# Performance work log

Measured on AMD Instinct MI355X. Metric: run time of the kernel, lower is better.

## Reference

```python
import jax, jax.numpy as jnp
import numpy as np

N = 262144   # nodes
E = 2097152  # edges (avg degree 8)
F_IN, L0, L1, K = 14, 128, 15, 15


def setup_inputs() -> dict:
    key = jax.random.key(0)
    ks = jax.random.split(key, 24)
    s = 0.1
    return {
        "x": jax.random.normal(ks[0], (N, F_IN), jnp.float32),
        "edge_index": jax.random.randint(ks[1], (2, E), 0, N, dtype=jnp.int32),
        "y": jax.random.randint(ks[2], (N, 1), 0, 2, dtype=jnp.int32),
        "sel": jax.random.bernoulli(ks[3], 0.98, (N, 1)),
        "Wl1": jax.random.normal(ks[4], (F_IN, L0)) * s,
        "Wr1": jax.random.normal(ks[5], (F_IN, L0)) * s,
        "b1": jnp.zeros((L0,), jnp.float32),
        "Wl2": jax.random.normal(ks[6], (L0, L0)) * s,
        "Wr2": jax.random.normal(ks[7], (L0, L0)) * s,
        "b2": jnp.zeros((L0,), jnp.float32),
        "Wl3": jax.random.normal(ks[8], (L0, 1)) * s,
        "Wr3": jax.random.normal(ks[9], (L0, 1)) * s,
        "b3": jnp.zeros((1,), jnp.float32),
        "Wt1": jax.random.normal(ks[10], (K + 1, F_IN, L1)) * s,
        "bt1": jnp.zeros((L1,), jnp.float32),
        "Wt2": jax.random.normal(ks[11], (K + 1, L1, L1)) * s,
        "bt2": jnp.zeros((L1,), jnp.float32),
        "Wt3": jax.random.normal(ks[12], (K + 1, L1, 1)) * s,
        "bt3": jnp.zeros((1,), jnp.float32),
        "Wlin": jax.random.normal(ks[13], (2, 1)) * s,
        "blin": jnp.zeros((1,), jnp.float32),
    }


def _sage(h, src, dst, inv_deg, Wl, Wr, b):
    # PyG SAGEConv (mean aggr): lin_l(mean_j x_j) + lin_r(x_i) + b
    agg = jax.ops.segment_sum(h[src], dst, num_segments=N) * inv_deg
    return agg @ Wl + h @ Wr + b


def _tag(h, src, dst, norm, W, b):
    # PyG TAGConv: sum_k (D^-1/2 A D^-1/2)^k x @ W_k + b
    out = h @ W[0]
    for k in range(1, W.shape[0]):
        h = jax.ops.segment_sum(norm[:, None] * h[src], dst, num_segments=N)
        out = out + h @ W[k]
    return out + b


def reference(x, edge_index, y, sel, Wl1, Wr1, b1, Wl2, Wr2, b2, Wl3, Wr3, b3,
              Wt1, bt1, Wt2, bt2, Wt3, bt3, Wlin, blin):
    src, dst = edge_index[0], edge_index[1]
    ones = jnp.ones((E,), jnp.float32)
    deg = jax.ops.segment_sum(ones, dst, num_segments=N)  # in-degree at targets
    inv_deg = (1.0 / jnp.maximum(deg, 1.0))[:, None]
    # gcn_norm without self-loops for TAGConv
    dinv = jnp.where(deg > 0, jax.lax.rsqrt(jnp.maximum(deg, 1.0)), 0.0)
    norm = dinv[src] * dinv[dst]  # [E]

    # SAGE branch
    x1 = jax.nn.sigmoid(_sage(x, src, dst, inv_deg, Wl1, Wr1, b1))
    for _ in range(4):
        x1 = jax.nn.sigmoid(_sage(x1, src, dst, inv_deg, Wl2, Wr2, b2))
    x1 = jax.nn.relu(_sage(x1, src, dst, inv_deg, Wl3, Wr3, b3))

    # TAG branch
    x3 = jax.nn.sigmoid(_tag(x, src, dst, norm, Wt1, bt1))
    for _ in range(4):
        x3 = jax.nn.sigmoid(_tag(x3, src, dst, norm, Wt2, bt2))
    x3 = jax.nn.relu(_tag(x3, src, dst, norm, Wt3, bt3))

    out = jax.nn.relu(jnp.concatenate([x1, x3], axis=1) @ Wlin + blin)
    return jnp.where(sel & (y == 0), 0.0, out)
```

## Files before the change

kernel.cpp:

```cpp
#include <hip/hip_runtime.h>
#include <math.h>

#define NN 262144
#define EE 2097152
#define FIN 14
#define LW 128
#define TW 15

typedef unsigned short ushort_t;
typedef unsigned int uint_t;
typedef __attribute__((ext_vector_type(8))) short bf16x8v;
typedef __attribute__((ext_vector_type(4))) float f32x4v;

static __device__ __forceinline__ float sigmoidf_(float v) { return 1.0f / (1.0f + expf(-v)); }

static __device__ __forceinline__ float bf2f(unsigned short u) {
  union { unsigned int i; float f; } v; v.i = ((unsigned int)u) << 16; return v.f;
}
static __device__ __forceinline__ unsigned short f2bf(float f) {
  union { float f; unsigned int i; } v; v.f = f;
  unsigned int r = v.i + 0x7FFF + ((v.i >> 16) & 1);
  return (unsigned short)(r >> 16);
}
static __device__ __forceinline__ unsigned int pack2(float a, float b) {
  return ((unsigned int)f2bf(b) << 16) | (unsigned int)f2bf(a);
}
static __device__ __forceinline__ void addrow16(float* acc, uint4 u0, uint4 u1) {
  acc[0]  += bf2f((unsigned short)(u0.x & 0xFFFF)); acc[1]  += bf2f((unsigned short)(u0.x >> 16));
  acc[2]  += bf2f((unsigned short)(u0.y & 0xFFFF)); acc[3]  += bf2f((unsigned short)(u0.y >> 16));
  acc[4]  += bf2f((unsigned short)(u0.z & 0xFFFF)); acc[5]  += bf2f((unsigned short)(u0.z >> 16));
  acc[6]  += bf2f((unsigned short)(u0.w & 0xFFFF)); acc[7]  += bf2f((unsigned short)(u0.w >> 16));
  acc[8]  += bf2f((unsigned short)(u1.x & 0xFFFF)); acc[9]  += bf2f((unsigned short)(u1.x >> 16));
  acc[10] += bf2f((unsigned short)(u1.y & 0xFFFF)); acc[11] += bf2f((unsigned short)(u1.y >> 16));
  acc[12] += bf2f((unsigned short)(u1.z & 0xFFFF)); acc[13] += bf2f((unsigned short)(u1.z >> 16));
  acc[14] += bf2f((unsigned short)(u1.w & 0xFFFF)); acc[15] += bf2f((unsigned short)(u1.w >> 16));
}

__global__ void k_selprobe(const unsigned char* __restrict__ selb, int* __restrict__ flag) {
  __shared__ int cnt;
  if (threadIdx.x == 0) cnt = 0;
  __syncthreads();
  int c = 0;
  for (int i = threadIdx.x; i < 4096; i += 256) c += (selb[i] != 0) ? 1 : 0;
  atomicAdd(&cnt, c);
  __syncthreads();
  if (threadIdx.x == 0) *flag = (cnt > 3000) ? 1 : 0;
}

__global__ void k_norm_bool(const int* __restrict__ flag, const unsigned char* __restrict__ selb,
                            unsigned char* __restrict__ selN) {
  if (*flag != 1) return;
  int i = blockIdx.x * 256 + threadIdx.x;
  selN[i] = (selb[i] != 0) ? 1 : 0;
}

__global__ void k_norm_int(const int* __restrict__ flag, const unsigned char* __restrict__ selb,
                           unsigned char* __restrict__ selN) {
  if (*flag != 0) return;
  int i = blockIdx.x * 256 + threadIdx.x;
  selN[i] = (((const int*)selb)[i] != 0) ? 1 : 0;
}

__global__ void k_deg(const int* __restrict__ ei, int* __restrict__ deg) {
  int e = blockIdx.x * 256 + threadIdx.x;
  if (e < EE) atomicAdd(&deg[ei[EE + e]], 1);
}

__global__ void k_scan_partial(const int* __restrict__ deg, int* __restrict__ btot) {
  __shared__ int sd[256];
  int t = threadIdx.x, b = blockIdx.x;
  int i0 = b * 1024 + t * 4;
  int s = deg[i0] + deg[i0 + 1] + deg[i0 + 2] + deg[i0 + 3];
  sd[t] = s; __syncthreads();
  for (int off = 1; off < 256; off <<= 1) {
    int x = (t >= off) ? sd[t - off] : 0;
    __syncthreads(); sd[t] += x; __syncthreads();
  }
  if (t == 255) btot[b] = sd[255];
}

__global__ void k_scan_block(const int* __restrict__ btot, int* __restrict__ bbase, int* __restrict__ row_start) {
  __shared__ int sd[256];
  int t = threadIdx.x;
  int v = btot[t];
  sd[t] = v; __syncthreads();
  for (int off = 1; off < 256; off <<= 1) {
    int x = (t >= off) ? sd[t - off] : 0;
    __syncthreads(); sd[t] += x; __syncthreads();
  }
  bbase[t] = sd[t] - v;
  if (t == 255) row_start[NN] = sd[255];
}

__global__ void k_scan_final(const int* __restrict__ deg, const int* __restrict__ bbase,
                             int* __restrict__ row_start, float* __restrict__ inv_deg,
                             float* __restrict__ dinv) {
  __shared__ int sd[256];
  int t = threadIdx.x, b = blockIdx.x;
  int i0 = b * 1024 + t * 4;
  int d0 = deg[i0], d1 = deg[i0 + 1], d2 = deg[i0 + 2], d3 = deg[i0 + 3];
  int s = d0 + d1 + d2 + d3;
  sd[t] = s; __syncthreads();
  for (int off = 1; off < 256; off <<= 1) {
    int x = (t >= off) ? sd[t - off] : 0;
    __syncthreads(); sd[t] += x; __syncthreads();
  }
  int base = bbase[b] + sd[t] - s;
  row_start[i0]     = base;
  row_start[i0 + 1] = base + d0;
  row_start[i0 + 2] = base + d0 + d1;
  row_start[i0 + 3] = base + d0 + d1 + d2;
  int dd[4] = {d0, d1, d2, d3};
  for (int j = 0; j < 4; ++j) {
    float df = (float)dd[j];
    inv_deg[i0 + j] = 1.0f / fmaxf(df, 1.0f);
    dinv[i0 + j] = (dd[j] > 0) ? rsqrtf(fmaxf(df, 1.0f)) : 0.0f;
  }
}

__global__ void k_fill(const int* __restrict__ ei, const int* __restrict__ row_start,
                       int* __restrict__ cursor, int* __restrict__ csr_src) {
  int e = blockIdx.x * 256 + threadIdx.x;
  if (e >= EE) return;
  int s = ei[e], d = ei[EE + e];
  int pos = atomicAdd(&cursor[d], 1);
  csr_src[row_start[d] + pos] = s;
}

__global__ void k_pad_x(const float* __restrict__ x, float* __restrict__ xp,
                        ushort_t* __restrict__ xpb) {
  int idx = blockIdx.x * 256 + threadIdx.x;
  int i = idx >> 4, lane = idx & 15;
  float v = (lane < FIN) ? x[(size_t)i * FIN + lane] : 0.0f;
  xp[idx] = v;
  xpb[idx] = f2bf(v);
}

__global__ __launch_bounds__(256) void k_prop16_mean(
    const float* __restrict__ h, float* __restrict__ out,
    const int* __restrict__ row_start, const int* __restrict__ csr_src,
    const float* __restrict__ inv_deg) {
  int i = blockIdx.x * 256 + threadIdx.x;
  float acc[16];
  #pragma unroll
  for (int c = 0; c < 16; ++c) acc[c] = 0.0f;
  int e0 = row_start[i], e1 = row_start[i + 1];
  int e = e0;
  for (; e + 2 <= e1; e += 2) {
    int i0 = csr_src[e], i1 = csr_src[e + 1];
    const float4* r0 = (const float4*)(h + (size_t)i0 * 16);
    const float4* r1 = (const float4*)(h + (size_t)i1 * 16);
    float4 a0 = r0[0], a1 = r0[1], a2 = r0[2], a3 = r0[3];
    float4 b0 = r1[0], b1 = r1[1], b2 = r1[2], b3 = r1[3];
    acc[0]+=a0.x+b0.x; acc[1]+=a0.y+b0.y; acc[2]+=a0.z+b0.z; acc[3]+=a0.w+b0.w;
    acc[4]+=a1.x+b1.x; acc[5]+=a1.y+b1.y; acc[6]+=a1.z+b1.z; acc[7]+=a1.w+b1.w;
    acc[8]+=a2.x+b2.x; acc[9]+=a2.y+b2.y; acc[10]+=a2.z+b2.z; acc[11]+=a2.w+b2.w;
    acc[12]+=a3.x+b3.x; acc[13]+=a3.y+b3.y; acc[14]+=a3.z+b3.z; acc[15]+=a3.w+b3.w;
  }
  for (; e < e1; ++e) {
    const float4* r0 = (const float4*)(h + (size_t)csr_src[e] * 16);
    float4 a0 = r0[0], a1 = r0[1], a2 = r0[2], a3 = r0[3];
    acc[0]+=a0.x; acc[1]+=a0.y; acc[2]+=a0.z; acc[3]+=a0.w;
    acc[4]+=a1.x; acc[5]+=a1.y; acc[6]+=a1.z; acc[7]+=a1.w;
    acc[8]+=a2.x; acc[9]+=a2.y; acc[10]+=a2.z; acc[11]+=a2.w;
    acc[12]+=a3.x; acc[13]+=a3.y; acc[14]+=a3.z; acc[15]+=a3.w;
  }
  float idg = inv_deg[i];
  float4 o[4];
  #pragma unroll
  for (int q = 0; q < 4; ++q) {
    o[q].x = acc[q*4+0]*idg; o[q].y = acc[q*4+1]*idg;
    o[q].z = acc[q*4+2]*idg; o[q].w = acc[q*4+3]*idg;
  }
  float4* dst = (float4*)(out + (size_t)i * 16);
  dst[0]=o[0]; dst[1]=o[1]; dst[2]=o[2]; dst[3]=o[3];
}

__global__ __launch_bounds__(256) void k_gemm_small(
    const float* __restrict__ A1, const float* __restrict__ A2,
    const float* __restrict__ W1, const float* __restrict__ W2,
    const float* __restrict__ bias, ushort_t* __restrict__ out) {
  __shared__ float W1s[FIN][LW];
  __shared__ float W2s[FIN][LW];
  int t = threadIdx.x;
  for (int idx = t; idx < FIN * LW; idx += 256) {
    W1s[idx / LW][idx % LW] = W1[idx];
    W2s[idx / LW][idx % LW] = W2[idx];
  }
  __syncthreads();
  int node = blockIdx.x * 4 + (t >> 6);
  int lane = t & 63;
  float a1 = (lane < 16) ? A1[(size_t)node * 16 + lane] : 0.0f;
  float a2 = (lane < 16) ? A2[(size_t)node * 16 + lane] : 0.0f;
  float acc0 = bias[lane], acc1 = bias[lane + 64];
  #pragma unroll
  for (int f = 0; f < FIN; ++f) {
    float v1 = __shfl(a1, f);
    float v2 = __shfl(a2, f);
    acc0 += v1 * W1s[f][lane]      + v2 * W2s[f][lane];
    acc1 += v1 * W1s[f][lane + 64] + v2 * W2s[f][lane + 64];
  }
  out[(size_t)node * LW + lane]      = f2bf(sigmoidf_(acc0));
  out[(size_t)node * LW + lane + 64] = f2bf(sigmoidf_(acc1));
}

__global__ void k_prop128(const ushort_t* __restrict__ h, ushort_t* __restrict__ out,
                          const int* __restrict__ row_start, const int* __restrict__ csr_src,
                          const float* __restrict__ inv_deg) {
  int t = threadIdx.x;
  int g = blockIdx.x * 4 + (t >> 6);
  int lane = t & 63;
  int s0 = row_start[g], s1 = row_start[g + 1];
  float a0 = 0.0f, a1 = 0.0f;
  int e = s0;
  for (; e + 4 <= s1; e += 4) {
    int i0 = csr_src[e], i1 = csr_src[e+1], i2 = csr_src[e+2], i3 = csr_src[e+3];
    uint_t u0 = *(const uint_t*)(h + (size_t)i0 * LW + 2 * lane);
    uint_t u1 = *(const uint_t*)(h + (size_t)i1 * LW + 2 * lane);
    uint_t u2 = *(const uint_t*)(h + (size_t)i2 * LW + 2 * lane);
    uint_t u3 = *(const uint_t*)(h + (size_t)i3 * LW + 2 * lane);
    a0 += bf2f((unsigned short)(u0 & 0xFFFF)) + bf2f((unsigned short)(u1 & 0xFFFF))
        + bf2f((unsigned short)(u2 & 0xFFFF)) + bf2f((unsigned short)(u3 & 0xFFFF));
    a1 += bf2f((unsigned short)(u0 >> 16)) + bf2f((unsigned short)(u1 >> 16))
        + bf2f((unsigned short)(u2 >> 16)) + bf2f((unsigned short)(u3 >> 16));
  }
  for (; e < s1; ++e) {
    uint_t u = *(const uint_t*)(h + (size_t)csr_src[e] * LW + 2 * lane);
    a0 += bf2f((unsigned short)(u & 0xFFFF));
    a1 += bf2f((unsigned short)(u >> 16));
  }
  float idg = inv_deg[g];
  *(uint_t*)(out + (size_t)g * LW + 2 * lane) = pack2(a0 * idg, a1 * idg);
}

__global__ void k_convW(const float* __restrict__ Wl, const float* __restrict__ Wr,
                        ushort_t* __restrict__ Wt) {
  int idx = blockIdx.x * 256 + threadIdx.x;
  int n = idx >> 8, k = idx & 255;
  float v = (k < 128) ? Wl[k * 128 + n] : Wr[(k - 128) * 128 + n];
  Wt[idx] = f2bf(v);
}

__global__ __launch_bounds__(256) void k_gemm128_mfma(
    const ushort_t* __restrict__ A1, const ushort_t* __restrict__ A2,
    const ushort_t* __restrict__ Wt,
    const float* __restrict__ bias, ushort_t* __restrict__ out) {
  int tid = threadIdx.x;
  int wave = tid >> 6, lane = tid & 63;
  int row0 = blockIdx.x * 64 + wave * 16;
  int r = lane & 15, kg = lane >> 4;
  f32x4v acc[8];
  #pragma unroll
  for (int nt = 0; nt < 8; ++nt) acc[nt] = (f32x4v){0.f, 0.f, 0.f, 0.f};
  #pragma unroll
  for (int ks = 0; ks < 8; ++ks) {
    const ushort_t* asrc = (ks < 4)
        ? (A1 + (size_t)(row0 + r) * LW + ks * 32 + kg * 8)
        : (A2 + (size_t)(row0 + r) * LW + (ks - 4) * 32 + kg * 8);
    bf16x8v a = *(const bf16x8v*)asrc;
    #pragma unroll
    for (int nt = 0; nt < 8; ++nt) {
      bf16x8v b = *(const bf16x8v*)(Wt + (size_t)(nt * 16 + r) * 256 + ks * 32 + kg * 8);
      acc[nt] = __builtin_amdgcn_mfma_f32_16x16x32_bf16(a, b, acc[nt], 0, 0, 0);
    }
  }
  #pragma unroll
  for (int nt = 0; nt < 8; ++nt) {
    #pragma unroll
    for (int j = 0; j < 4; ++j) {
      float v = sigmoidf_(acc[nt][j] + bias[nt * 16 + r]);
      out[(size_t)(row0 + kg * 4 + j) * LW + nt * 16 + r] = f2bf(v);
    }
  }
}

__global__ void k_wide_to1(const ushort_t* __restrict__ H, const float* __restrict__ Wl3,
                           const float* __restrict__ Wr3, float* __restrict__ g_l,
                           float* __restrict__ g_r) {
  int wave = (blockIdx.x * 256 + threadIdx.x) >> 6;
  int lane = threadIdx.x & 63;
  unsigned int u = *(const unsigned int*)(H + (size_t)wave * LW + 2 * lane);
  float h0 = bf2f((unsigned short)(u & 0xFFFF));
  float h1 = bf2f((unsigned short)(u >> 16));
  float al = h0 * Wl3[2 * lane] + h1 * Wl3[2 * lane + 1];
  float ar = h0 * Wr3[2 * lane] + h1 * Wr3[2 * lane + 1];
  #pragma unroll
  for (int off = 32; off; off >>= 1) {
    al += __shfl_xor(al, off);
    ar += __shfl_xor(ar, off);
  }
  if (lane == 0) { g_l[wave] = al; g_r[wave] = ar; }
}

__global__ void k_sage_final(const float* __restrict__ g_l, const float* __restrict__ g_r,
                             const float* __restrict__ b3, const int* __restrict__ row_start,
                             const int* __restrict__ csr_src, const float* __restrict__ inv_deg,
                             float* __restrict__ x1) {
  int i = blockIdx.x * 256 + threadIdx.x;
  int e0 = row_start[i], e1 = row_start[i + 1];
  float s = 0.0f;
  int e = e0;
  for (; e + 4 <= e1; e += 4) {
    float w0 = g_l[csr_src[e]], w1 = g_l[csr_src[e+1]];
    float w2 = g_l[csr_src[e+2]], w3 = g_l[csr_src[e+3]];
    s += (w0 + w1) + (w2 + w3);
  }
  for (; e < e1; ++e) s += g_l[csr_src[e]];
  float v = s * inv_deg[i] + g_r[i] + b3[0];
  x1[i] = fmaxf(v, 0.0f);
}

__global__ __launch_bounds__(256) void k_tag_hh(
    const ushort_t* __restrict__ T, const float* __restrict__ W, int win,
    const ushort_t* __restrict__ w_in, ushort_t* __restrict__ w_out,
    const float* __restrict__ bias, int mode,
    const int* __restrict__ row_start, const int* __restrict__ csr_src,
    const float* __restrict__ dinv) {
  __shared__ float Ws[16][16];
  int t = threadIdx.x;
  { int rr = t >> 4, c = t & 15; Ws[rr][c] = (rr < win && c < TW) ? W[rr * TW + c] : 0.0f; }
  __syncthreads();
  int i = blockIdx.x * 256 + t;
  float di = dinv[i];
  float acc[16];
  #pragma unroll
  for (int c = 0; c < 16; ++c) acc[c] = 0.0f;

  if (mode != 0) {
    int e0 = row_start[i], e1 = row_start[i + 1];
    int e = e0;
    for (; e + 4 <= e1; e += 4) {
      int i0 = csr_src[e], i1 = csr_src[e+1], i2 = csr_src[e+2], i3 = csr_src[e+3];
      uint4 a0 = *(const uint4*)(w_in + (size_t)i0 * 16);
      uint4 a1 = *(const uint4*)(w_in + (size_t)i0 * 16 + 8);
      uint4 b0 = *(const uint4*)(w_in + (size_t)i1 * 16);
      uint4 b1 = *(const uint4*)(w_in + (size_t)i1 * 16 + 8);
      uint4 c0 = *(const uint4*)(w_in + (size_t)i2 * 16);
      uint4 c1 = *(const uint4*)(w_in + (size_t)i2 * 16 + 8);
      uint4 d0 = *(const uint4*)(w_in + (size_t)i3 * 16);
      uint4 d1 = *(const uint4*)(w_in + (size_t)i3 * 16 + 8);
      addrow16(acc, a0, a1);
      addrow16(acc, b0, b1);
      addrow16(acc, c0, c1);
      addrow16(acc, d0, d1);
    }
    for (; e < e1; ++e) {
      int i0 = csr_src[e];
      uint4 a0 = *(const uint4*)(w_in + (size_t)i0 * 16);
      uint4 a1 = *(const uint4*)(w_in + (size_t)i0 * 16 + 8);
      addrow16(acc, a0, a1);
    }
    #pragma unroll
    for (int c = 0; c < 16; ++c) acc[c] *= di;
  }

  uint4 t0 = *(const uint4*)(T + (size_t)i * 16);
  uint4 t1 = *(const uint4*)(T + (size_t)i * 16 + 8);
  float tv[16];
  tv[0]=bf2f((unsigned short)(t0.x&0xFFFF)); tv[1]=bf2f((unsigned short)(t0.x>>16));
  tv[2]=bf2f((unsigned short)(t0.y&0xFFFF)); tv[3]=bf2f((unsigned short)(t0.y>>16));
  tv[4]=bf2f((unsigned short)(t0.z&0xFFFF)); tv[5]=bf2f((unsigned short)(t0.z>>16));
  tv[6]=bf2f((unsigned short)(t0.w&0xFFFF)); tv[7]=bf2f((unsigned short)(t0.w>>16));
  tv[8]=bf2f((unsigned short)(t1.x&0xFFFF)); tv[9]=bf2f((unsigned short)(t1.x>>16));
  tv[10]=bf2f((unsigned short)(t1.y&0xFFFF)); tv[11]=bf2f((unsigned short)(t1.y>>16));
  tv[12]=bf2f((unsigned short)(t1.z&0xFFFF)); tv[13]=bf2f((unsigned short)(t1.z>>16));
  tv[14]=bf2f((unsigned short)(t1.w&0xFFFF)); tv[15]=bf2f((unsigned short)(t1.w>>16));
  #pragma unroll
  for (int f = 0; f < 16; ++f) {
    float tf = tv[f];
    const float4* wr = (const float4*)Ws[f];
    float4 w0 = wr[0], w1 = wr[1], w2 = wr[2], w3 = wr[3];
    acc[0]+=tf*w0.x; acc[1]+=tf*w0.y; acc[2]+=tf*w0.z; acc[3]+=tf*w0.w;
    acc[4]+=tf*w1.x; acc[5]+=tf*w1.y; acc[6]+=tf*w1.z; acc[7]+=tf*w1.w;
    acc[8]+=tf*w2.x; acc[9]+=tf*w2.y; acc[10]+=tf*w2.z; acc[11]+=tf*w2.w;
    acc[12]+=tf*w3.x; acc[13]+=tf*w3.y; acc[14]+=tf*w3.z; acc[15]+=tf*w3.w;
  }

  uint_t o[8];
  if (mode == 2) {
    #pragma unroll
    for (int q = 0; q < 8; ++q) {
      float v0 = (2*q   < TW) ? sigmoidf_(acc[2*q]   + bias[2*q])   : 0.0f;
      float v1 = (2*q+1 < TW) ? sigmoidf_(acc[2*q+1] + bias[2*q+1]) : 0.0f;
      o[q] = pack2(v0, v1);
    }
  } else {
    #pragma unroll
    for (int q = 0; q < 8; ++q) o[q] = pack2(di * acc[2*q], di * acc[2*q+1]);
  }
  uint4* dst = (uint4*)(w_out + (size_t)i * 16);
  dst[0] = make_uint4(o[0], o[1], o[2], o[3]);
  dst[1] = make_uint4(o[4], o[5], o[6], o[7]);
}

__global__ void k_tag_g(const ushort_t* __restrict__ T, const float* __restrict__ Wt3,
                        float* __restrict__ gT) {
  __shared__ float Ws[16 * TW];
  int t = threadIdx.x;
  if (t < 16 * TW) Ws[t] = Wt3[t];
  __syncthreads();
  int i = blockIdx.x * 256 + t;
  const ushort_t* tr = T + (size_t)i * 16;
  float row[TW];
  #pragma unroll
  for (int f = 0; f < TW; ++f) row[f] = bf2f(tr[f]);
  #pragma unroll
  for (int k = 0; k < 16; ++k) {
    float a = 0.0f;
    #pragma unroll
    for (int f = 0; f < TW; ++f) a += row[f] * Ws[k * TW + f];
    gT[(size_t)k * NN + i] = a;
  }
}

__global__ void k_scale1(const float* __restrict__ g15, const float* __restrict__ dinv,
                         float* __restrict__ w) {
  int i = blockIdx.x * 256 + threadIdx.x;
  w[i] = dinv[i] * g15[i];
}

__global__ void k_horner(const float* __restrict__ gk, const float* __restrict__ w_in,
                         float* __restrict__ w_out, int last,
                         const int* __restrict__ row_start, const int* __restrict__ csr_src,
                         const float* __restrict__ dinv) {
  int i = blockIdx.x * 256 + threadIdx.x;
  int e0 = row_start[i], e1 = row_start[i + 1];
  float gs = 0.0f;
  int e = e0;
  for (; e + 4 <= e1; e += 4) {
    float w0 = w_in[csr_src[e]],   w1 = w_in[csr_src[e+1]];
    float w2 = w_in[csr_src[e+2]], w3 = w_in[csr_src[e+3]];
    gs += (w0 + w1) + (w2 + w3);
  }
  for (; e < e1; ++e) gs += w_in[csr_src[e]];
  float s = gk[i] + dinv[i] * gs;
  w_out[i] = last ? s : dinv[i] * s;
}

__global__ void k_combine(const float* __restrict__ x1, const float* __restrict__ s,
                          const int* __restrict__ y, const unsigned char* __restrict__ selN,
                          const float* __restrict__ Wlin, const float* __restrict__ blin,
                          const float* __restrict__ bt3, float* __restrict__ out) {
  int i = blockIdx.x * 256 + threadIdx.x;
  float x3 = fmaxf(s[i] + bt3[0], 0.0f);
  float v = fmaxf(x1[i] * Wlin[0] + x3 * Wlin[1] + blin[0], 0.0f);
  bool z = (selN[i] != 0) && (y[i] == 0);
  out[i] = z ? 0.0f : v;
}

extern "C" void kernel_launch(void* const* d_in, const int* in_sizes, int n_in,
                              void* d_out, int out_size, void* d_ws, size_t ws_size,
                              hipStream_t stream) {
  const float* x    = (const float*)d_in[0];
  const int*   ei   = (const int*)d_in[1];
  const int*   y    = (const int*)d_in[2];
  const unsigned char* sel = (const unsigned char*)d_in[3];
  const float* Wl1  = (const float*)d_in[4];
  const float* Wr1  = (const float*)d_in[5];
  const float* b1   = (const float*)d_in[6];
  const float* Wl2  = (const float*)d_in[7];
  const float* Wr2  = (const float*)d_in[8];
  const float* b2   = (const float*)d_in[9];
  const float* Wl3  = (const float*)d_in[10];
  const float* Wr3  = (const float*)d_in[11];
  const float* b3   = (const float*)d_in[12];
  const float* Wt1  = (const float*)d_in[13];
  const float* bt1  = (const float*)d_in[14];
  const float* Wt2  = (const float*)d_in[15];
  const float* bt2  = (const float*)d_in[16];
  const float* Wt3  = (const float*)d_in[17];
  const float* bt3  = (const float*)d_in[18];
  const float* Wlin = (const float*)d_in[19];
  const float* blin = (const float*)d_in[20];

  const size_t MB = 1 << 20;
  unsigned char* w8 = (unsigned char*)d_ws;
  int*   deg       = (int*)(w8 + 0 * MB);
  int*   cursor    = (int*)(w8 + 1 * MB);
  int*   row_start = (int*)(w8 + 2 * MB);
  float* inv_deg   = (float*)(w8 + 4 * MB);
  float* dinv      = (float*)(w8 + 5 * MB);
  float* x1        = (float*)(w8 + 6 * MB);
  float* g_l       = (float*)(w8 + 7 * MB);
  float* g_r       = (float*)(w8 + 8 * MB);
  int*   btot      = (int*)(w8 + 9 * MB);
  int*   bbase     = (int*)(w8 + 9 * MB + 4096);
  int*   selflag   = (int*)(w8 + 9 * MB + 8192);
  float* sA        = (float*)(w8 + 10 * MB);
  float* w6a       = (float*)(w8 + 11 * MB);
  float* w6b       = (float*)(w8 + 12 * MB);
  unsigned char* selN = (unsigned char*)(w8 + 13 * MB);
  ushort_t* Wtc    = (ushort_t*)(w8 + 14 * MB);
  int*   csr_src   = (int*)(w8 + 16 * MB);
  float* xp        = (float*)(w8 + 24 * MB);
  ushort_t* xpb    = (ushort_t*)(w8 + 40 * MB);
  ushort_t* H      = (ushort_t*)(w8 + 48 * MB);
  ushort_t* AGG    = (ushort_t*)(w8 + 112 * MB);
  float* agg16     = (float*)(w8 + 112 * MB);
  ushort_t* T0  = (ushort_t*)(w8 + 112 * MB);
  ushort_t* T1  = (ushort_t*)(w8 + 120 * MB);
  ushort_t* wA  = (ushort_t*)(w8 + 128 * MB);
  ushort_t* wB  = (ushort_t*)(w8 + 136 * MB);
  float* gT     = (float*)(w8 + 144 * MB);

  k_selprobe<<<1, 256, 0, stream>>>(sel, selflag);
  k_norm_bool<<<NN / 256, 256, 0, stream>>>(selflag, sel, selN);
  k_norm_int<<<NN / 256, 256, 0, stream>>>(selflag, sel, selN);

  hipMemsetAsync(w8, 0, 2 * MB, stream);
  k_deg<<<EE / 256, 256, 0, stream>>>(ei, deg);
  k_scan_partial<<<256, 256, 0, stream>>>(deg, btot);
  k_scan_block<<<1, 256, 0, stream>>>(btot, bbase, row_start);
  k_scan_final<<<256, 256, 0, stream>>>(deg, bbase, row_start, inv_deg, dinv);
  k_fill<<<EE / 256, 256, 0, stream>>>(ei, row_start, cursor, csr_src);
  k_pad_x<<<NN * 16 / 256, 256, 0, stream>>>(x, xp, xpb);
  k_convW<<<128, 256, 0, stream>>>(Wl2, Wr2, Wtc);

  k_prop16_mean<<<NN / 256, 256, 0, stream>>>(xp, agg16, row_start, csr_src, inv_deg);
  k_gemm_small<<<NN / 4, 256, 0, stream>>>(agg16, xp, Wl1, Wr1, b1, H);
  for (int l = 0; l < 4; ++l) {
    k_prop128<<<NN / 4, 256, 0, stream>>>(H, AGG, row_start, csr_src, inv_deg);
    k_gemm128_mfma<<<NN / 64, 256, 0, stream>>>(AGG, H, Wtc, b2, H);
  }
  k_wide_to1<<<NN / 4, 256, 0, stream>>>(H, Wl3, Wr3, g_l, g_r);
  k_sage_final<<<NN / 256, 256, 0, stream>>>(g_l, g_r, b3, row_start, csr_src, inv_deg, x1);

  {
    const ushort_t* T = xpb;
    k_tag_hh<<<NN / 256, 256, 0, stream>>>(T, Wt1 + (size_t)15 * FIN * TW, FIN,
                                           nullptr, wA, nullptr, 0, row_start, csr_src, dinv);
    ushort_t* wi = wA; ushort_t* wo = wB;
    for (int k = 14; k >= 1; --k) {
      k_tag_hh<<<NN / 256, 256, 0, stream>>>(T, Wt1 + (size_t)k * FIN * TW, FIN,
                                             wi, wo, nullptr, 1, row_start, csr_src, dinv);
      ushort_t* tmp = wi; wi = wo; wo = tmp;
    }
    k_tag_hh<<<NN / 256, 256, 0, stream>>>(T, Wt1, FIN, wi, T0, bt1, 2,
                                           row_start, csr_src, dinv);
  }
  ushort_t* tin = T0; ushort_t* tout = T1;
  for (int l = 0; l < 4; ++l) {
    k_tag_hh<<<NN / 256, 256, 0, stream>>>(tin, Wt2 + (size_t)15 * TW * TW, TW,
                                           nullptr, wA, nullptr, 0, row_start, csr_src, dinv);
    ushort_t* wi = wA; ushort_t* wo = wB;
    for (int k = 14; k >= 1; --k) {
      k_tag_hh<<<NN / 256, 256, 0, stream>>>(tin, Wt2 + (size_t)k * TW * TW, TW,
                                             wi, wo, nullptr, 1, row_start, csr_src, dinv);
      ushort_t* tmp = wi; wi = wo; wo = tmp;
    }
    k_tag_hh<<<NN / 256, 256, 0, stream>>>(tin, Wt2, TW, wi, tout, bt2, 2,
                                           row_start, csr_src, dinv);
    ushort_t* tmp = tin; tin = tout; tout = tmp;
  }
  k_tag_g<<<NN / 256, 256, 0, stream>>>(tin, Wt3, gT);
  k_scale1<<<NN / 256, 256, 0, stream>>>(gT + (size_t)15 * NN, dinv, w6a);
  float* wi = w6a; float* wo = w6b;
  for (int k = 14; k >= 0; --k) {
    int last = (k == 0) ? 1 : 0;
    float* dst = last ? sA : wo;
    k_horner<<<NN / 256, 256, 0, stream>>>(gT + (size_t)k * NN, wi, dst, last,
                                           row_start, csr_src, dinv);
    float* tmp = wi; wi = wo; wo = tmp;
  }

  k_combine<<<NN / 256, 256, 0, stream>>>(x1, sA, y, selN, Wlin, blin, bt3, (float*)d_out);
}
```

Before: 4.211 ms.

## Fuse TAG layer boundaries, Horner tail, and use MFMA for first SAGE layer

Several changes at once. The first SAGE layer's aggregate and self features are packed into one bf16 buffer so a single MFMA GEMM replaces the shared-memory FMA GEMM, and the gather loops in prop128 and tag_hh are unrolled to 8 edges to keep more loads in flight. Each TAG layer's final kernel also computes the next layer's k=15 Horner seed, which removes one launch per layer. k_scale1 is folded into k_tag_g and the last Horner step into the combine kernel. The price is extra register pressure and a bf16-rounded agg input to the first GEMM.

```diff
diff --git a/kernel.cpp b/kernel.cpp
--- a/kernel.cpp
+++ b/kernel.cpp
@@ -128,16 +128,18 @@
 }
 
 __global__ void k_pad_x(const float* __restrict__ x, float* __restrict__ xp,
-                        ushort_t* __restrict__ xpb) {
+                        ushort_t* __restrict__ xpb, ushort_t* __restrict__ xc) {
   int idx = blockIdx.x * 256 + threadIdx.x;
   int i = idx >> 4, lane = idx & 15;
   float v = (lane < FIN) ? x[(size_t)i * FIN + lane] : 0.0f;
   xp[idx] = v;
-  xpb[idx] = f2bf(v);
+  ushort_t b = f2bf(v);
+  xpb[idx] = b;
+  xc[(size_t)i * 32 + 16 + lane] = b;
 }
 
 __global__ __launch_bounds__(256) void k_prop16_mean(
-    const float* __restrict__ h, float* __restrict__ out,
+    const float* __restrict__ h, ushort_t* __restrict__ xc,
     const int* __restrict__ row_start, const int* __restrict__ csr_src,
     const float* __restrict__ inv_deg) {
   int i = blockIdx.x * 256 + threadIdx.x;
@@ -166,42 +168,47 @@
     acc[12]+=a3.x; acc[13]+=a3.y; acc[14]+=a3.z; acc[15]+=a3.w;
   }
   float idg = inv_deg[i];
-  float4 o[4];
-  #pragma unroll
-  for (int q = 0; q < 4; ++q) {
-    o[q].x = acc[q*4+0]*idg; o[q].y = acc[q*4+1]*idg;
-    o[q].z = acc[q*4+2]*idg; o[q].w = acc[q*4+3]*idg;
-  }
-  float4* dst = (float4*)(out + (size_t)i * 16);
-  dst[0]=o[0]; dst[1]=o[1]; dst[2]=o[2]; dst[3]=o[3];
-}
-
-__global__ __launch_bounds__(256) void k_gemm_small(
-    const float* __restrict__ A1, const float* __restrict__ A2,
-    const float* __restrict__ W1, const float* __restrict__ W2,
+  uint_t o[8];
+  #pragma unroll
+  for (int q = 0; q < 8; ++q) o[q] = pack2(acc[2*q]*idg, acc[2*q+1]*idg);
+  uint4* dst = (uint4*)(xc + (size_t)i * 32);
+  dst[0] = make_uint4(o[0], o[1], o[2], o[3]);
+  dst[1] = make_uint4(o[4], o[5], o[6], o[7]);
+}
+
+__global__ void k_convW1(const float* __restrict__ Wl1, const float* __restrict__ Wr1,
+                         ushort_t* __restrict__ Wc) {
+  int idx = blockIdx.x * 256 + threadIdx.x;
+  int n = idx >> 5, k = idx & 31;
+  float v = 0.0f;
+  if (k < FIN) v = Wl1[k * 128 + n];
+  else if (k >= 16 && k < 16 + FIN) v = Wr1[(k - 16) * 128 + n];
+  Wc[idx] = f2bf(v);
+}
+
+__global__ __launch_bounds__(256) void k_gemm_small_mfma(
+    const ushort_t* __restrict__ xc, const ushort_t* __restrict__ Wc,
     const float* __restrict__ bias, ushort_t* __restrict__ out) {
-  __shared__ float W1s[FIN][LW];
-  __shared__ float W2s[FIN][LW];
-  int t = threadIdx.x;
-  for (int idx = t; idx < FIN * LW; idx += 256) {
-    W1s[idx / LW][idx % LW] = W1[idx];
-    W2s[idx / LW][idx % LW] = W2[idx];
-  }
-  __syncthreads();
-  int node = blockIdx.x * 4 + (t >> 6);
-  int lane = t & 63;
-  float a1 = (lane < 16) ? A1[(size_t)node * 16 + lane] : 0.0f;
-  float a2 = (lane < 16) ? A2[(size_t)node * 16 + lane] : 0.0f;
-  float acc0 = bias[lane], acc1 = bias[lane + 64];
-  #pragma unroll
-  for (int f = 0; f < FIN; ++f) {
-    float v1 = __shfl(a1, f);
-    float v2 = __shfl(a2, f);
-    acc0 += v1 * W1s[f][lane]      + v2 * W2s[f][lane];
-    acc1 += v1 * W1s[f][lane + 64] + v2 * W2s[f][lane + 64];
-  }
-  out[(size_t)node * LW + lane]      = f2bf(sigmoidf_(acc0));
-  out[(size_t)node * LW + lane + 64] = f2bf(sigmoidf_(acc1));
+  int tid = threadIdx.x;
+  int wave = tid >> 6, lane = tid & 63;
+  int row0 = blockIdx.x * 64 + wave * 16;
+  int r = lane & 15, kg = lane >> 4;
+  bf16x8v a = *(const bf16x8v*)(xc + (size_t)(row0 + r) * 32 + kg * 8);
+  f32x4v acc[8];
+  #pragma unroll
+  for (int nt = 0; nt < 8; ++nt) {
+    acc[nt] = (f32x4v){0.f, 0.f, 0.f, 0.f};
+    bf16x8v b = *(const bf16x8v*)(Wc + (size_t)(nt * 16 + r) * 32 + kg * 8);
+    acc[nt] = __builtin_amdgcn_mfma_f32_16x16x32_bf16(a, b, acc[nt], 0, 0, 0);
+  }
+  #pragma unroll
+  for (int nt = 0; nt < 8; ++nt) {
+    #pragma unroll
+    for (int j = 0; j < 4; ++j) {
+      float v = sigmoidf_(acc[nt][j] + bias[nt * 16 + r]);
+      out[(size_t)(row0 + kg * 4 + j) * LW + nt * 16 + r] = f2bf(v);
+    }
+  }
 }
 
 __global__ void k_prop128(const ushort_t* __restrict__ h, ushort_t* __restrict__ out,
@@ -213,16 +220,18 @@
   int s0 = row_start[g], s1 = row_start[g + 1];
   float a0 = 0.0f, a1 = 0.0f;
   int e = s0;
-  for (; e + 4 <= s1; e += 4) {
-    int i0 = csr_src[e], i1 = csr_src[e+1], i2 = csr_src[e+2], i3 = csr_src[e+3];
-    uint_t u0 = *(const uint_t*)(h + (size_t)i0 * LW + 2 * lane);
-    uint_t u1 = *(const uint_t*)(h + (size_t)i1 * LW + 2 * lane);
-    uint_t u2 = *(const uint_t*)(h + (size_t)i2 * LW + 2 * lane);
-    uint_t u3 = *(const uint_t*)(h + (size_t)i3 * LW + 2 * lane);
-    a0 += bf2f((unsigned short)(u0 & 0xFFFF)) + bf2f((unsigned short)(u1 & 0xFFFF))
-        + bf2f((unsigned short)(u2 & 0xFFFF)) + bf2f((unsigned short)(u3 & 0xFFFF));
-    a1 += bf2f((unsigned short)(u0 >> 16)) + bf2f((unsigned short)(u1 >> 16))
-        + bf2f((unsigned short)(u2 >> 16)) + bf2f((unsigned short)(u3 >> 16));
+  for (; e + 8 <= s1; e += 8) {
+    int id[8];
+    #pragma unroll
+    for (int j = 0; j < 8; ++j) id[j] = csr_src[e + j];
+    uint_t u[8];
+    #pragma unroll
+    for (int j = 0; j < 8; ++j) u[j] = *(const uint_t*)(h + (size_t)id[j] * LW + 2 * lane);
+    #pragma unroll
+    for (int j = 0; j < 8; ++j) {
+      a0 += bf2f((unsigned short)(u[j] & 0xFFFF));
+      a1 += bf2f((unsigned short)(u[j] >> 16));
+    }
   }
   for (; e < s1; ++e) {
     uint_t u = *(const uint_t*)(h + (size_t)csr_src[e] * LW + 2 * lane);
@@ -314,11 +323,17 @@
     const ushort_t* __restrict__ T, const float* __restrict__ W, int win,
     const ushort_t* __restrict__ w_in, ushort_t* __restrict__ w_out,
     const float* __restrict__ bias, int mode,
+    const float* __restrict__ W2, int win2, ushort_t* __restrict__ w_next2,
     const int* __restrict__ row_start, const int* __restrict__ csr_src,
     const float* __restrict__ dinv) {
   __shared__ float Ws[16][16];
+  __shared__ float Ws2[16][16];
   int t = threadIdx.x;
   { int rr = t >> 4, c = t & 15; Ws[rr][c] = (rr < win && c < TW) ? W[rr * TW + c] : 0.0f; }
+  if (mode == 3) {
+    int rr = t >> 4, c = t & 15;
+    Ws2[rr][c] = (rr < win2 && c < TW) ? W2[rr * TW + c] : 0.0f;
+  }
   __syncthreads();
   int i = blockIdx.x * 256 + t;
   float di = dinv[i];
@@ -329,26 +344,35 @@
   if (mode != 0) {
     int e0 = row_start[i], e1 = row_start[i + 1];
     int e = e0;
+    for (; e + 8 <= e1; e += 8) {
+      int id[8];
+      #pragma unroll
+      for (int j = 0; j < 8; ++j) id[j] = csr_src[e + j];
+      uint4 u0[8], u1[8];
+      #pragma unroll
+      for (int j = 0; j < 8; ++j) {
+        const uint4* p = (const uint4*)(w_in + (size_t)id[j] * 16);
+        u0[j] = p[0]; u1[j] = p[1];
+      }
+      #pragma unroll
+      for (int j = 0; j < 8; ++j) addrow16(acc, u0[j], u1[j]);
+    }
     for (; e + 4 <= e1; e += 4) {
-      int i0 = csr_src[e], i1 = csr_src[e+1], i2 = csr_src[e+2], i3 = csr_src[e+3];
-      uint4 a0 = *(const uint4*)(w_in + (size_t)i0 * 16);
-      uint4 a1 = *(const uint4*)(w_in + (size_t)i0 * 16 + 8);
-      uint4 b0 = *(const uint4*)(w_in + (size_t)i1 * 16);
-      uint4 b1 = *(const uint4*)(w_in + (size_t)i1 * 16 + 8);
-      uint4 c0 = *(const uint4*)(w_in + (size_t)i2 * 16);
-      uint4 c1 = *(const uint4*)(w_in + (size_t)i2 * 16 + 8);
-      uint4 d0 = *(const uint4*)(w_in + (size_t)i3 * 16);
-      uint4 d1 = *(const uint4*)(w_in + (size_t)i3 * 16 + 8);
-      addrow16(acc, a0, a1);
-      addrow16(acc, b0, b1);
-      addrow16(acc, c0, c1);
-      addrow16(acc, d0, d1);
+      int id[4];
+      #pragma unroll
+      for (int j = 0; j < 4; ++j) id[j] = csr_src[e + j];
+      uint4 u0[4], u1[4];
+      #pragma unroll
+      for (int j = 0; j < 4; ++j) {
+        const uint4* p = (const uint4*)(w_in + (size_t)id[j] * 16);
+        u0[j] = p[0]; u1[j] = p[1];
+      }
+      #pragma unroll
+      for (int j = 0; j < 4; ++j) addrow16(acc, u0[j], u1[j]);
     }
     for (; e < e1; ++e) {
-      int i0 = csr_src[e];
-      uint4 a0 = *(const uint4*)(w_in + (size_t)i0 * 16);
-      uint4 a1 = *(const uint4*)(w_in + (size_t)i0 * 16 + 8);
-      addrow16(acc, a0, a1);
+      const uint4* p = (const uint4*)(w_in + (size_t)csr_src[e] * 16);
+      addrow16(acc, p[0], p[1]);
     }
     #pragma unroll
     for (int c = 0; c < 16; ++c) acc[c] *= di;
@@ -376,25 +400,51 @@
     acc[12]+=tf*w3.x; acc[13]+=tf*w3.y; acc[14]+=tf*w3.z; acc[15]+=tf*w3.w;
   }
 
-  uint_t o[8];
-  if (mode == 2) {
-    #pragma unroll
-    for (int q = 0; q < 8; ++q) {
-      float v0 = (2*q   < TW) ? sigmoidf_(acc[2*q]   + bias[2*q])   : 0.0f;
-      float v1 = (2*q+1 < TW) ? sigmoidf_(acc[2*q+1] + bias[2*q+1]) : 0.0f;
-      o[q] = pack2(v0, v1);
+  if (mode >= 2) {
+    float tn[16];
+    #pragma unroll
+    for (int c = 0; c < 16; ++c)
+      tn[c] = (c < TW) ? sigmoidf_(acc[c] + bias[c]) : 0.0f;
+    uint_t o[8];
+    #pragma unroll
+    for (int q = 0; q < 8; ++q) o[q] = pack2(tn[2*q], tn[2*q+1]);
+    uint4* dst = (uint4*)(w_out + (size_t)i * 16);
+    dst[0] = make_uint4(o[0], o[1], o[2], o[3]);
+    dst[1] = make_uint4(o[4], o[5], o[6], o[7]);
+    if (mode == 3) {
+      float wn[16];
+      #pragma unroll
+      for (int c = 0; c < 16; ++c) wn[c] = 0.0f;
+      #pragma unroll
+      for (int f = 0; f < 16; ++f) {
+        float tf = tn[f];
+        const float4* wr = (const float4*)Ws2[f];
+        float4 w0 = wr[0], w1 = wr[1], w2 = wr[2], w3 = wr[3];
+        wn[0]+=tf*w0.x; wn[1]+=tf*w0.y; wn[2]+=tf*w0.z; wn[3]+=tf*w0.w;
+        wn[4]+=tf*w1.x; wn[5]+=tf*w1.y; wn[6]+=tf*w1.z; wn[7]+=tf*w1.w;
+        wn[8]+=tf*w2.x; wn[9]+=tf*w2.y; wn[10]+=tf*w2.z; wn[11]+=tf*w2.w;
+        wn[12]+=tf*w3.x; wn[13]+=tf*w3.y; wn[14]+=tf*w3.z; wn[15]+=tf*w3.w;
+      }
+      uint_t o2[8];
+      #pragma unroll
+      for (int q = 0; q < 8; ++q) o2[q] = pack2(di * wn[2*q], di * wn[2*q+1]);
+      uint4* dst2 = (uint4*)(w_next2 + (size_t)i * 16);
+      dst2[0] = make_uint4(o2[0], o2[1], o2[2], o2[3]);
+      dst2[1] = make_uint4(o2[4], o2[5], o2[6], o2[7]);
     }
   } else {
+    uint_t o[8];
     #pragma unroll
     for (int q = 0; q < 8; ++q) o[q] = pack2(di * acc[2*q], di * acc[2*q+1]);
-  }
-  uint4* dst = (uint4*)(w_out + (size_t)i * 16);
-  dst[0] = make_uint4(o[0], o[1], o[2], o[3]);
-  dst[1] = make_uint4(o[4], o[5], o[6], o[7]);
+    uint4* dst = (uint4*)(w_out + (size_t)i * 16);
+    dst[0] = make_uint4(o[0], o[1], o[2], o[3]);
+    dst[1] = make_uint4(o[4], o[5], o[6], o[7]);
+  }
 }
 
 __global__ void k_tag_g(const ushort_t* __restrict__ T, const float* __restrict__ Wt3,
-                        float* __restrict__ gT) {
+                        const float* __restrict__ dinv, float* __restrict__ gT,
+                        float* __restrict__ w15) {
   __shared__ float Ws[16 * TW];
   int t = threadIdx.x;
   if (t < 16 * TW) Ws[t] = Wt3[t];
@@ -409,18 +459,13 @@
     float a = 0.0f;
     #pragma unroll
     for (int f = 0; f < TW; ++f) a += row[f] * Ws[k * TW + f];
-    gT[(size_t)k * NN + i] = a;
-  }
-}
-
-__global__ void k_scale1(const float* __restrict__ g15, const float* __restrict__ dinv,
-                         float* __restrict__ w) {
-  int i = blockIdx.x * 256 + threadIdx.x;
-  w[i] = dinv[i] * g15[i];
+    if (k < 15) gT[(size_t)k * NN + i] = a;
+    else        w15[i] = dinv[i] * a;
+  }
 }
 
 __global__ void k_horner(const float* __restrict__ gk, const float* __restrict__ w_in,
-                         float* __restrict__ w_out, int last,
+                         float* __restrict__ w_out,
                          const int* __restrict__ row_start, const int* __restrict__ csr_src,
                          const float* __restrict__ dinv) {
   int i = blockIdx.x * 256 + threadIdx.x;
@@ -434,15 +479,28 @@
   }
   for (; e < e1; ++e) gs += w_in[csr_src[e]];
   float s = gk[i] + dinv[i] * gs;
-  w_out[i] = last ? s : dinv[i] * s;
-}
-
-__global__ void k_combine(const float* __restrict__ x1, const float* __restrict__ s,
-                          const int* __restrict__ y, const unsigned char* __restrict__ selN,
-                          const float* __restrict__ Wlin, const float* __restrict__ blin,
-                          const float* __restrict__ bt3, float* __restrict__ out) {
+  w_out[i] = dinv[i] * s;
+}
+
+__global__ void k_horner_fin(const float* __restrict__ g0, const float* __restrict__ w_in,
+                             const float* __restrict__ x1, const int* __restrict__ y,
+                             const unsigned char* __restrict__ selN,
+                             const float* __restrict__ Wlin, const float* __restrict__ blin,
+                             const float* __restrict__ bt3,
+                             const int* __restrict__ row_start, const int* __restrict__ csr_src,
+                             const float* __restrict__ dinv, float* __restrict__ out) {
   int i = blockIdx.x * 256 + threadIdx.x;
-  float x3 = fmaxf(s[i] + bt3[0], 0.0f);
+  int e0 = row_start[i], e1 = row_start[i + 1];
+  float gs = 0.0f;
+  int e = e0;
+  for (; e + 4 <= e1; e += 4) {
+    float w0 = w_in[csr_src[e]],   w1 = w_in[csr_src[e+1]];
+    float w2 = w_in[csr_src[e+2]], w3 = w_in[csr_src[e+3]];
+    gs += (w0 + w1) + (w2 + w3);
+  }
+  for (; e < e1; ++e) gs += w_in[csr_src[e]];
+  float s = g0[i] + dinv[i] * gs;
+  float x3 = fmaxf(s + bt3[0], 0.0f);
   float v = fmaxf(x1[i] * Wlin[0] + x3 * Wlin[1] + blin[0], 0.0f);
   bool z = (selN[i] != 0) && (y[i] == 0);
   out[i] = z ? 0.0f : v;
@@ -486,17 +544,17 @@
   int*   btot      = (int*)(w8 + 9 * MB);
   int*   bbase     = (int*)(w8 + 9 * MB + 4096);
   int*   selflag   = (int*)(w8 + 9 * MB + 8192);
-  float* sA        = (float*)(w8 + 10 * MB);
   float* w6a       = (float*)(w8 + 11 * MB);
   float* w6b       = (float*)(w8 + 12 * MB);
   unsigned char* selN = (unsigned char*)(w8 + 13 * MB);
   ushort_t* Wtc    = (ushort_t*)(w8 + 14 * MB);
+  ushort_t* Wc1    = (ushort_t*)(w8 + 15 * MB);
   int*   csr_src   = (int*)(w8 + 16 * MB);
   float* xp        = (float*)(w8 + 24 * MB);
   ushort_t* xpb    = (ushort_t*)(w8 + 40 * MB);
   ushort_t* H      = (ushort_t*)(w8 + 48 * MB);
   ushort_t* AGG    = (ushort_t*)(w8 + 112 * MB);
-  float* agg16     = (float*)(w8 + 112 * MB);
+  ushort_t* xc     = (ushort_t*)(w8 + 112 * MB);
   ushort_t* T0  = (ushort_t*)(w8 + 112 * MB);
   ushort_t* T1  = (ushort_t*)(w8 + 120 * MB);
   ushort_t* wA  = (ushort_t*)(w8 + 128 * MB);
@@ -513,11 +571,12 @@
   k_scan_block<<<1, 256, 0, stream>>>(btot, bbase, row_start);
   k_scan_final<<<256, 256, 0, stream>>>(deg, bbase, row_start, inv_deg, dinv);
   k_fill<<<EE / 256, 256, 0, stream>>>(ei, row_start, cursor, csr_src);
-  k_pad_x<<<NN * 16 / 256, 256, 0, stream>>>(x, xp, xpb);
+  k_pad_x<<<NN * 16 / 256, 256, 0, stream>>>(x, xp, xpb, xc);
   k_convW<<<128, 256, 0, stream>>>(Wl2, Wr2, Wtc);
-
-  k_prop16_mean<<<NN / 256, 256, 0, stream>>>(xp, agg16, row_start, csr_src, inv_deg);
-  k_gemm_small<<<NN / 4, 256, 0, stream>>>(agg16, xp, Wl1, Wr1, b1, H);
+  k_convW1<<<16, 256, 0, stream>>>(Wl1, Wr1, Wc1);
+
+  k_prop16_mean<<<NN / 256, 256, 0, stream>>>(xp, xc, row_start, csr_src, inv_deg);
+  k_gemm_small_mfma<<<NN / 64, 256, 0, stream>>>(xc, Wc1, b1, H);
   for (int l = 0; l < 4; ++l) {
     k_prop128<<<NN / 4, 256, 0, stream>>>(H, AGG, row_start, csr_src, inv_deg);
     k_gemm128_mfma<<<NN / 64, 256, 0, stream>>>(AGG, H, Wtc, b2, H);
@@ -525,43 +584,43 @@
   k_wide_to1<<<NN / 4, 256, 0, stream>>>(H, Wl3, Wr3, g_l, g_r);
   k_sage_final<<<NN / 256, 256, 0, stream>>>(g_l, g_r, b3, row_start, csr_src, inv_deg, x1);
 
-  {
-    const ushort_t* T = xpb;
-    k_tag_hh<<<NN / 256, 256, 0, stream>>>(T, Wt1 + (size_t)15 * FIN * TW, FIN,
-                                           nullptr, wA, nullptr, 0, row_start, csr_src, dinv);
-    ushort_t* wi = wA; ushort_t* wo = wB;
-    for (int k = 14; k >= 1; --k) {
-      k_tag_hh<<<NN / 256, 256, 0, stream>>>(T, Wt1 + (size_t)k * FIN * TW, FIN,
-                                             wi, wo, nullptr, 1, row_start, csr_src, dinv);
-      ushort_t* tmp = wi; wi = wo; wo = tmp;
-    }
-    k_tag_hh<<<NN / 256, 256, 0, stream>>>(T, Wt1, FIN, wi, T0, bt1, 2,
-                                           row_start, csr_src, dinv);
-  }
+  const size_t FT = (size_t)FIN * TW;
+  const size_t TT = (size_t)TW * TW;
+  ushort_t* wi = wA; ushort_t* wo = wB;
+  k_tag_hh<<<NN / 256, 256, 0, stream>>>(xpb, Wt1 + 15 * FT, FIN, nullptr, wi, nullptr, 0,
+                                         nullptr, 0, nullptr, row_start, csr_src, dinv);
+  for (int k = 14; k >= 1; --k) {
+    k_tag_hh<<<NN / 256, 256, 0, stream>>>(xpb, Wt1 + (size_t)k * FT, FIN, wi, wo, nullptr, 1,
+                                           nullptr, 0, nullptr, row_start, csr_src, dinv);
+    ushort_t* tmp = wi; wi = wo; wo = tmp;
+  }
+  k_tag_hh<<<NN / 256, 256, 0, stream>>>(xpb, Wt1, FIN, wi, T0, bt1, 3,
+                                         Wt2 + 15 * TT, TW, wo, row_start, csr_src, dinv);
+  { ushort_t* tmp = wi; wi = wo; wo = tmp; }
   ushort_t* tin = T0; ushort_t* tout = T1;
   for (int l = 0; l < 4; ++l) {
-    k_tag_hh<<<NN / 256, 256, 0, stream>>>(tin, Wt2 + (size_t)15 * TW * TW, TW,
-                                           nullptr, wA, nullptr, 0, row_start, csr_src, dinv);
-    ushort_t* wi = wA; ushort_t* wo = wB;
     for (int k = 14; k >= 1; --k) {
-      k_tag_hh<<<NN / 256, 256, 0, stream>>>(tin, Wt2 + (size_t)k * TW * TW, TW,
-                                             wi, wo, nullptr, 1, row_start, csr_src, dinv);
+      k_tag_hh<<<NN / 256, 256, 0, stream>>>(tin, Wt2 + (size_t)k * TT, TW, wi, wo, nullptr, 1,
+                                             nullptr, 0, nullptr, row_start, csr_src, dinv);
       ushort_t* tmp = wi; wi = wo; wo = tmp;
     }
-    k_tag_hh<<<NN / 256, 256, 0, stream>>>(tin, Wt2, TW, wi, tout, bt2, 2,
+    if (l < 3) {
+      k_tag_hh<<<NN / 256, 256, 0, stream>>>(tin, Wt2, TW, wi, tout, bt2, 3,
+                                             Wt2 + 15 * TT, TW, wo, row_start, csr_src, dinv);
+      ushort_t* tmp = wi; wi = wo; wo = tmp;
+    } else {
+      k_tag_hh<<<NN / 256, 256, 0, stream>>>(tin, Wt2, TW, wi, tout, bt2, 2,
+                                             nullptr, 0, nullptr, row_start, csr_src, dinv);
+    }
+    ushort_t* tmp = tin; tin = tout; tout = tmp;
+  }
+  k_tag_g<<<NN / 256, 256, 0, stream>>>(tin, Wt3, dinv, gT, w6a);
+  float* fwi = w6a; float* fwo = w6b;
+  for (int k = 14; k >= 1; --k) {
+    k_horner<<<NN / 256, 256, 0, stream>>>(gT + (size_t)k * NN, fwi, fwo,
                                            row_start, csr_src, dinv);
-    ushort_t* tmp = tin; tin = tout; tout = tmp;
-  }
-  k_tag_g<<<NN / 256, 256, 0, stream>>>(tin, Wt3, gT);
-  k_scale1<<<NN / 256, 256, 0, stream>>>(gT + (size_t)15 * NN, dinv, w6a);
-  float* wi = w6a; float* wo = w6b;
-  for (int k = 14; k >= 0; --k) {
-    int last = (k == 0) ? 1 : 0;
-    float* dst = last ? sA : wo;
-    k_horner<<<NN / 256, 256, 0, stream>>>(gT + (size_t)k * NN, wi, dst, last,
-                                           row_start, csr_src, dinv);
-    float* tmp = wi; wi = wo; wo = tmp;
-  }
-
-  k_combine<<<NN / 256, 256, 0, stream>>>(x1, sA, y, selN, Wlin, blin, bt3, (float*)d_out);
-}
+    float* tmp = fwi; fwi = fwo; fwo = tmp;
+  }
+  k_horner_fin<<<NN / 256, 256, 0, stream>>>(gT, fwi, x1, y, selN, Wlin, blin, bt3,
+                                             row_start, csr_src, dinv, (float*)d_out);
+}
```

Result: slower. 4.309 ms (+2.3%).
